# Kernel tuning notes

Hardware: AMD Instinct MI355X
Metric: run time of the kernel (lower is better)

The kernel has to match this reference:

```python
import jax, jax.numpy as jnp
import numpy as np

N_NODES = 100000
N_EDGES = 600000
N_CLASS = 26
HIDDEN = 128


def setup_inputs() -> dict:
    key = jax.random.key(0)
    ks = jax.random.split(key, 8)
    x = jax.random.normal(ks[0], (N_NODES, N_CLASS), dtype=jnp.float32)
    edge_index = jax.random.randint(ks[1], (2, N_EDGES), 0, N_NODES, dtype=jnp.int64)
    edge_weight = jax.random.uniform(ks[2], (N_EDGES,), dtype=jnp.float32)
    W1 = jax.random.normal(ks[3], (N_CLASS, HIDDEN), dtype=jnp.float32) * (1.0 / np.sqrt(N_CLASS))
    b1 = jnp.zeros((HIDDEN,), dtype=jnp.float32)
    W2 = jax.random.normal(ks[4], (HIDDEN, HIDDEN), dtype=jnp.float32) * (1.0 / np.sqrt(HIDDEN))
    b2 = jnp.zeros((HIDDEN,), dtype=jnp.float32)
    Wfc = jax.random.normal(ks[5], (HIDDEN, N_CLASS), dtype=jnp.float32) * (1.0 / np.sqrt(HIDDEN))
    bfc = jnp.zeros((N_CLASS,), dtype=jnp.float32)
    return {"x": x, "edge_index": edge_index, "edge_weight": edge_weight,
            "W1": W1, "b1": b1, "W2": W2, "b2": b2, "Wfc": Wfc, "bfc": bfc}


def _gcn_norm(edge_index, edge_weight, n_nodes):
    # PyG gcn_norm: add self-loops (weight 1), symmetric deg^-1/2 normalization.
    loop = jnp.arange(n_nodes, dtype=edge_index.dtype)
    row = jnp.concatenate([edge_index[0], loop])  # source
    col = jnp.concatenate([edge_index[1], loop])  # destination
    w = jnp.concatenate([edge_weight, jnp.ones((n_nodes,), edge_weight.dtype)])
    deg = jax.ops.segment_sum(w, col, num_segments=n_nodes)
    d_inv_sqrt = jnp.where(deg > 0, jax.lax.rsqrt(jnp.maximum(deg, 1e-12)), 0.0)
    norm = d_inv_sqrt[row] * w * d_inv_sqrt[col]
    return row, col, norm


def _gcn_conv(x, row, col, norm, W, b, n_nodes):
    h = x @ W                              # [N, out]
    msg = norm[:, None] * h[row]           # gather + scale, [E+N, out]
    out = jax.ops.segment_sum(msg, col, num_segments=n_nodes)  # scatter-add
    return out + b


def reference(x, edge_index, edge_weight, W1, b1, W2, b2, Wfc, bfc):
    n = x.shape[0]
    row, col, norm = _gcn_norm(edge_index, edge_weight, n)
    h = jax.nn.relu(_gcn_conv(x, row, col, norm, W1, b1, n))
    h = jax.nn.relu(_gcn_conv(h, row, col, norm, W2, b2, n))
    return h @ Wfc + bfc
```

## Files before the change

### kernel.cpp

```cpp
#include <hip/hip_runtime.h>

#define NNODES 100000
#define NEDGES 600000
#define NCLASS 26
#define HID    128

#define SHIFT  9
#define BCOLS  512
#define NBKT   196
#define EPB    1024
#define NBE    586
#define NH     (NBKT * NBE)

typedef __attribute__((ext_vector_type(8))) short bf16x8;
typedef __attribute__((ext_vector_type(4))) float f32x4;

__device__ inline unsigned short f2bf(float f) {
    unsigned int u = __float_as_uint(f);
    u += 0x7fffu + ((u >> 16) & 1u);
    return (unsigned short)(u >> 16);
}
__device__ inline unsigned int packbf(float a, float b) {
    return (unsigned int)f2bf(a) | ((unsigned int)f2bf(b) << 16);
}
__device__ inline float2 bfpair(unsigned int p) {
    float2 r;
    r.x = __uint_as_float(p << 16);
    r.y = __uint_as_float(p & 0xffff0000u);
    return r;
}
__device__ inline void fma8(float* a, float w, uint4 g) {
    float2 p;
    p = bfpair(g.x); a[0] = fmaf(w, p.x, a[0]); a[1] = fmaf(w, p.y, a[1]);
    p = bfpair(g.y); a[2] = fmaf(w, p.x, a[2]); a[3] = fmaf(w, p.y, a[3]);
    p = bfpair(g.z); a[4] = fmaf(w, p.x, a[4]); a[5] = fmaf(w, p.y, a[5]);
    p = bfpair(g.w); a[6] = fmaf(w, p.x, a[6]); a[7] = fmaf(w, p.y, a[7]);
}
__device__ inline void set8(float* a, uint4 g) {
    float2 p;
    p = bfpair(g.x); a[0] = p.x; a[1] = p.y;
    p = bfpair(g.y); a[2] = p.x; a[3] = p.y;
    p = bfpair(g.z); a[4] = p.x; a[5] = p.y;
    p = bfpair(g.w); a[6] = p.x; a[7] = p.y;
}

__global__ __launch_bounds__(256) void histA_k(const int* __restrict__ col,
                                               int* __restrict__ H) {
    __shared__ int h[NBKT];
    int t = threadIdx.x;
    for (int i = t; i < NBKT; i += 256) h[i] = 0;
    __syncthreads();
    int base = blockIdx.x * EPB;
#pragma unroll
    for (int u = 0; u < 4; u++) {
        int e = base + t + u * 256;
        if (e < NEDGES) atomicAdd(&h[col[e] >> SHIFT], 1);
    }
    __syncthreads();
    for (int i = t; i < NBKT; i += 256) H[i * NBE + blockIdx.x] = h[i];
}

__global__ void scanH1_k(const int* __restrict__ in, int* __restrict__ incl,
                         int* __restrict__ aux, int n) {
    __shared__ int s[256];
    int t = threadIdx.x, gi = blockIdx.x * 256 + t;
    s[t] = (gi < n) ? in[gi] : 0;
    __syncthreads();
    for (int off = 1; off < 256; off <<= 1) {
        int x = (t >= off) ? s[t - off] : 0;
        __syncthreads();
        s[t] += x;
        __syncthreads();
    }
    if (gi < n) incl[gi] = s[t];
    if (t == 255) aux[blockIdx.x] = s[255];
}

__global__ void scan2_k(int* __restrict__ aux, int n) {
    __shared__ int s[512];
    int t = threadIdx.x;
    s[t] = (t < n) ? aux[t] : 0;
    __syncthreads();
    for (int off = 1; off < 512; off <<= 1) {
        int x = (t >= off) ? s[t - off] : 0;
        __syncthreads();
        s[t] += x;
        __syncthreads();
    }
    if (t < n) aux[t] = s[t];
}

__device__ inline int exoff(const int* __restrict__ incl, const int* __restrict__ H,
                            const int* __restrict__ aux, int gi) {
    int add = (gi >= 256) ? aux[(gi >> 8) - 1] : 0;
    return incl[gi] - H[gi] + add;
}

__global__ __launch_bounds__(256) void partB_k(const int* __restrict__ row,
                                               const int* __restrict__ col,
                                               const float* __restrict__ w,
                                               const int* __restrict__ incl,
                                               const int* __restrict__ H,
                                               const int* __restrict__ aux,
                                               uint2* __restrict__ rw,
                                               unsigned short* __restrict__ lc) {
    __shared__ int off[NBKT];
    __shared__ int cur[NBKT];
    int t = threadIdx.x;
    for (int i = t; i < NBKT; i += 256) {
        off[i] = exoff(incl, H, aux, i * NBE + blockIdx.x);
        cur[i] = 0;
    }
    __syncthreads();
    int base = blockIdx.x * EPB;
#pragma unroll
    for (int u = 0; u < 4; u++) {
        int e = base + t + u * 256;
        if (e < NEDGES) {
            int c = col[e], b = c >> SHIFT;
            int p = off[b] + atomicAdd(&cur[b], 1);
            rw[p] = make_uint2((unsigned int)row[e], __float_as_uint(w[e]));
            lc[p] = (unsigned short)(c & (BCOLS - 1));
        }
    }
}

__global__ __launch_bounds__(256) void segbp_k(const uint2* __restrict__ rw,
                                               const unsigned short* __restrict__ lc,
                                               const int* __restrict__ incl,
                                               const int* __restrict__ H,
                                               const int* __restrict__ aux,
                                               int* __restrict__ rowptr,
                                               float* __restrict__ dis,
                                               uint2* __restrict__ meta) {
    __shared__ int   cnt[BCOLS];
    __shared__ float ws[BCOLS];
    __shared__ int   rpl[BCOLS];
    __shared__ int   ps[256];
    int b = blockIdx.x, t = threadIdx.x;
    int c0 = b << SHIFT;
    int ncols = min(BCOLS, NNODES - c0);
    for (int i = t; i < BCOLS; i += 256) { cnt[i] = 0; ws[i] = 0.f; }
    __syncthreads();
    int s    = exoff(incl, H, aux, b * NBE);
    int eend = (b == NBKT - 1) ? NEDGES : exoff(incl, H, aux, (b + 1) * NBE);
    for (int e = s + t; e < eend; e += 256) {
        uint2 m = rw[e];
        int l = lc[e];
        atomicAdd(&cnt[l], 1);
        atomicAdd(&ws[l], __uint_as_float(m.y));
    }
    __syncthreads();
    for (int i = t; i < ncols; i += 256) dis[c0 + i] = rsqrtf(1.0f + ws[i]);
    int a0 = cnt[2 * t], a1 = cnt[2 * t + 1];
    ps[t] = a0 + a1;
    __syncthreads();
    for (int off = 1; off < 256; off <<= 1) {
        int x = (t >= off) ? ps[t - off] : 0;
        __syncthreads();
        ps[t] += x;
        __syncthreads();
    }
    int ex = (t > 0) ? ps[t - 1] : 0;
    rpl[2 * t]     = s + ex;
    rpl[2 * t + 1] = s + ex + a0;
    if (2 * t     < ncols) rowptr[c0 + 2 * t]     = s + ex;
    if (2 * t + 1 < ncols) rowptr[c0 + 2 * t + 1] = s + ex + a0;
    if (b == NBKT - 1 && t == 0) rowptr[NNODES] = NEDGES;
    cnt[2 * t] = 0; cnt[2 * t + 1] = 0;
    __syncthreads();
    for (int e = s + t; e < eend; e += 256) {
        uint2 m = rw[e];
        int l = lc[e];
        int pos = rpl[l] + atomicAdd(&cnt[l], 1);
        meta[pos] = make_uint2(m.x, m.y);
    }
}

__global__ __launch_bounds__(256) void prep_k(const float* __restrict__ W2,
                                              const float* __restrict__ W1,
                                              const float* __restrict__ Wfc,
                                              const float* __restrict__ x,
                                              const float* __restrict__ dis,
                                              unsigned short* __restrict__ wt,
                                              unsigned short* __restrict__ w1t,
                                              unsigned short* __restrict__ wfct,
                                              unsigned int* __restrict__ xp) {
    int b = blockIdx.x, t = threadIdx.x;
    if (b < 64) {
        int idx = b * 256 + t;
        int c = idx >> 7, k = idx & 127;
        wt[c * 128 + k] = f2bf(W2[k * 128 + c]);
    } else if (b < 80) {
        int idx = (b - 64) * 256 + t;
        int c = idx >> 5, k = idx & 31;
        w1t[c * 32 + k] = (k < NCLASS) ? f2bf(W1[k * 128 + c]) : (unsigned short)0;
    } else if (b < 96) {
        int idx = (b - 80) * 256 + t;
        int c = idx >> 7, k = idx & 127;
        wfct[c * 128 + k] = (c < NCLASS) ? f2bf(Wfc[k * NCLASS + c]) : (unsigned short)0;
    } else {
        int i = (b - 96) * 256 + t;
        if (i < NNODES * 16) {
            int r = i >> 4, u = i & 15, f0 = u * 2;
            float d = dis[r];
            float a = (f0     < NCLASS) ? x[r * NCLASS + f0]     : 0.f;
            float c = (f0 + 1 < NCLASS) ? x[r * NCLASS + f0 + 1] : 0.f;
            xp[i] = packbf(d * a, d * c);
        }
    }
}

__global__ __launch_bounds__(256) void agg26_k(const int* __restrict__ rowptr,
                                               const uint2* __restrict__ meta,
                                               const unsigned int* __restrict__ xp,
                                               const float* __restrict__ dis,
                                               unsigned int* __restrict__ aggx) {
    int node = blockIdx.x * 16 + (threadIdx.x >> 4);
    int lane = threadIdx.x & 15;

    float2 acc = bfpair(xp[node * 16 + lane]);
    int j = rowptr[node], jend = rowptr[node + 1];
    for (; j + 3 < jend; j += 4) {
        uint2 m0 = meta[j],     m1 = meta[j + 1];
        uint2 m2 = meta[j + 2], m3 = meta[j + 3];
        unsigned int g0 = xp[m0.x * 16 + lane];
        unsigned int g1 = xp[m1.x * 16 + lane];
        unsigned int g2 = xp[m2.x * 16 + lane];
        unsigned int g3 = xp[m3.x * 16 + lane];
        float v0 = __uint_as_float(m0.y), v1 = __uint_as_float(m1.y);
        float v2 = __uint_as_float(m2.y), v3 = __uint_as_float(m3.y);
        float2 a;
        a = bfpair(g0); acc.x = fmaf(v0, a.x, acc.x); acc.y = fmaf(v0, a.y, acc.y);
        a = bfpair(g1); acc.x = fmaf(v1, a.x, acc.x); acc.y = fmaf(v1, a.y, acc.y);
        a = bfpair(g2); acc.x = fmaf(v2, a.x, acc.x); acc.y = fmaf(v2, a.y, acc.y);
        a = bfpair(g3); acc.x = fmaf(v3, a.x, acc.x); acc.y = fmaf(v3, a.y, acc.y);
    }
    for (; j < jend; j++) {
        uint2 m = meta[j];
        float v = __uint_as_float(m.y);
        float2 a = bfpair(xp[m.x * 16 + lane]);
        acc.x = fmaf(v, a.x, acc.x); acc.y = fmaf(v, a.y, acc.y);
    }
    float d = dis[node];
    aggx[node * 16 + lane] = packbf(d * acc.x, d * acc.y);
}

__global__ __launch_bounds__(256) void gemm12_k(const unsigned short* __restrict__ aggx,
                                                const unsigned short* __restrict__ w1t,
                                                const float* __restrict__ b1,
                                                const unsigned short* __restrict__ wt,
                                                const float* __restrict__ dis,
                                                unsigned short* __restrict__ C, int N) {
    __shared__ unsigned short h1s[128 * 136];
    __shared__ unsigned short Ws[128 * 72];
    const int tid  = threadIdx.x;
    const int wave = tid >> 6, lane = tid & 63;
    const int quad = lane >> 4, l16 = lane & 15;
    const int wm = wave >> 1, wn = wave & 1;
    const int row0 = blockIdx.x * 128;

    bf16x8 a1[4], bw1[4];
#pragma unroll
    for (int t = 0; t < 4; t++) {
        int r = row0 + wm * 64 + t * 16 + l16;
        a1[t] = (r < N) ? *(const bf16x8*)&aggx[(size_t)r * 32 + quad * 8]
                        : (bf16x8)(short)0;
        bw1[t] = *(const bf16x8*)&w1t[(wn * 64 + t * 16 + l16) * 32 + quad * 8];
    }
#pragma unroll
    for (int jj = 0; jj < 4; jj++) {
        int idx = tid + jj * 256;
        int r = idx >> 3, ku = idx & 7;
        *(uint4*)&Ws[r * 72 + ku * 8] = *(const uint4*)&wt[(size_t)r * 128 + ku * 8];
    }
    float b1v[4];
#pragma unroll
    for (int tn = 0; tn < 4; tn++) b1v[tn] = b1[wn * 64 + tn * 16 + l16];
#pragma unroll
    for (int tm = 0; tm < 4; tm++) {
#pragma unroll
        for (int tn = 0; tn < 4; tn++) {
            f32x4 hacc = __builtin_amdgcn_mfma_f32_16x16x32_bf16(
                a1[tm], bw1[tn], (f32x4)0.f, 0, 0, 0);
            int rl = wm * 64 + tm * 16 + quad * 4;
            int col = wn * 64 + tn * 16 + l16;
#pragma unroll
            for (int r = 0; r < 4; r++)
                h1s[(rl + r) * 136 + col] = f2bf(fmaxf(hacc[r] + b1v[tn], 0.f));
        }
    }
    __syncthreads();

    f32x4 acc[4][4];
#pragma unroll
    for (int i = 0; i < 4; i++)
#pragma unroll
        for (int j = 0; j < 4; j++) acc[i][j] = (f32x4)0.f;

    for (int c = 0; c < 2; c++) {
        if (c == 1) {
            __syncthreads();
#pragma unroll
            for (int jj = 0; jj < 4; jj++) {
                int idx = tid + jj * 256;
                int r = idx >> 3, ku = idx & 7;
                *(uint4*)&Ws[r * 72 + ku * 8] =
                    *(const uint4*)&wt[(size_t)r * 128 + 64 + ku * 8];
            }
            __syncthreads();
        }
#pragma unroll
        for (int kc = 0; kc < 2; kc++) {
            const int klA = c * 64 + kc * 32 + quad * 8;
            const int klW = kc * 32 + quad * 8;
            bf16x8 af[4], bfr[4];
#pragma unroll
            for (int t = 0; t < 4; t++) {
                af[t]  = *(const bf16x8*)&h1s[(wm * 64 + t * 16 + l16) * 136 + klA];
                bfr[t] = *(const bf16x8*)&Ws[(wn * 64 + t * 16 + l16) * 72 + klW];
            }
#pragma unroll
            for (int tm = 0; tm < 4; tm++)
#pragma unroll
                for (int tn = 0; tn < 4; tn++)
                    acc[tm][tn] = __builtin_amdgcn_mfma_f32_16x16x32_bf16(
                        af[tm], bfr[tn], acc[tm][tn], 0, 0, 0);
        }
    }

#pragma unroll
    for (int tm = 0; tm < 4; tm++) {
        const int rbase = row0 + wm * 64 + tm * 16 + quad * 4;
        float dv[4];
#pragma unroll
        for (int r = 0; r < 4; r++)
            dv[r] = (rbase + r < N) ? dis[rbase + r] : 0.f;
#pragma unroll
        for (int tn = 0; tn < 4; tn++) {
            const int col = wn * 64 + tn * 16 + l16;
#pragma unroll
            for (int r = 0; r < 4; r++) {
                if (rbase + r < N)
                    C[(size_t)(rbase + r) * 128 + col] = f2bf(dv[r] * acc[tm][tn][r]);
            }
        }
    }
}

__global__ __launch_bounds__(256) void aggfc_k(const int* __restrict__ rowptr,
                                               const uint2* __restrict__ meta,
                                               const unsigned short* __restrict__ h,
                                               const float* __restrict__ dis,
                                               const float* __restrict__ b2,
                                               const unsigned short* __restrict__ wfct,
                                               const float* __restrict__ bfc,
                                               float* __restrict__ out, int N) {
    const int tid = threadIdx.x;
    const int wv = tid >> 6, lane = tid & 63;
    const int q = lane >> 4, m = lane & 15;
    const int nbase = blockIdx.x * 64 + wv * 16;
    const int node = nbase + m;
    const bool valid = node < N;

    float acc[4][8];
    if (valid) {
        const uint4* self = (const uint4*)&h[(size_t)node * 128];
#pragma unroll
        for (int ks = 0; ks < 4; ks++) set8(acc[ks], self[ks * 4 + q]);
    } else {
#pragma unroll
        for (int ks = 0; ks < 4; ks++)
#pragma unroll
            for (int jj = 0; jj < 8; jj++) acc[ks][jj] = 0.f;
    }

    int j = valid ? rowptr[node] : 0;
    int jend = valid ? rowptr[node + 1] : 0;
    for (; j + 1 < jend; j += 2) {
        uint2 m0 = meta[j], m1 = meta[j + 1];
        const uint4* s0 = (const uint4*)&h[(size_t)m0.x * 128];
        const uint4* s1 = (const uint4*)&h[(size_t)m1.x * 128];
        uint4 g0[4], g1[4];
#pragma unroll
        for (int ks = 0; ks < 4; ks++) { g0[ks] = s0[ks * 4 + q]; g1[ks] = s1[ks * 4 + q]; }
        float w0 = __uint_as_float(m0.y), w1 = __uint_as_float(m1.y);
#pragma unroll
        for (int ks = 0; ks < 4; ks++) { fma8(acc[ks], w0, g0[ks]); fma8(acc[ks], w1, g1[ks]); }
    }
    if (j < jend) {
        uint2 mt = meta[j];
        const uint4* s0 = (const uint4*)&h[(size_t)mt.x * 128];
        float w0 = __uint_as_float(mt.y);
#pragma unroll
        for (int ks = 0; ks < 4; ks++) fma8(acc[ks], w0, s0[ks * 4 + q]);
    }

    float d = valid ? dis[node] : 0.f;
    bf16x8 af[4];
#pragma unroll
    for (int ks = 0; ks < 4; ks++) {
        const float4* bp = (const float4*)&b2[ks * 32 + q * 8];
        float4 bA = bp[0], bB = bp[1];
        union { bf16x8 v; unsigned short s[8]; } u;
        u.s[0] = f2bf(fmaxf(fmaf(d, acc[ks][0], bA.x), 0.f));
        u.s[1] = f2bf(fmaxf(fmaf(d, acc[ks][1], bA.y), 0.f));
        u.s[2] = f2bf(fmaxf(fmaf(d, acc[ks][2], bA.z), 0.f));
        u.s[3] = f2bf(fmaxf(fmaf(d, acc[ks][3], bA.w), 0.f));
        u.s[4] = f2bf(fmaxf(fmaf(d, acc[ks][4], bB.x), 0.f));
        u.s[5] = f2bf(fmaxf(fmaf(d, acc[ks][5], bB.y), 0.f));
        u.s[6] = f2bf(fmaxf(fmaf(d, acc[ks][6], bB.z), 0.f));
        u.s[7] = f2bf(fmaxf(fmaf(d, acc[ks][7], bB.w), 0.f));
        af[ks] = u.v;
    }

#pragma unroll
    for (int n = 0; n < 2; n++) {
        f32x4 o = (f32x4)0.f;
#pragma unroll
        for (int ks = 0; ks < 4; ks++) {
            bf16x8 bfr = *(const bf16x8*)&wfct[(size_t)(n * 16 + m) * 128 + ks * 32 + q * 8];
            o = __builtin_amdgcn_mfma_f32_16x16x32_bf16(af[ks], bfr, o, 0, 0, 0);
        }
        int col = n * 16 + m;
        if (col < NCLASS) {
            float bv = bfc[col];
            int r0 = nbase + q * 4;
#pragma unroll
            for (int r = 0; r < 4; r++) {
                if (r0 + r < N)
                    out[(size_t)(r0 + r) * NCLASS + col] = o[r] + bv;
            }
        }
    }
}

extern "C" void kernel_launch(void* const* d_in, const int* in_sizes, int n_in,
                              void* d_out, int out_size, void* d_ws, size_t ws_size,
                              hipStream_t stream) {
    const float* x   = (const float*)d_in[0];
    const int*   ei  = (const int*)d_in[1];
    const float* ew  = (const float*)d_in[2];
    const float* W1  = (const float*)d_in[3];
    const float* b1  = (const float*)d_in[4];
    const float* W2  = (const float*)d_in[5];
    const float* b2  = (const float*)d_in[6];
    const float* Wfc = (const float*)d_in[7];
    const float* bfc = (const float*)d_in[8];
    float* out = (float*)d_out;

    const int N = NNODES;
    const int* erow = ei;
    const int* ecol = ei + NEDGES;

    float* fws    = (float*)d_ws;
    float* dis    = fws;
    int*   rowptr = (int*)(fws + 100000);
    int*   H      = (int*)(fws + 200004);
    int*   incl   = (int*)(fws + 314860);
    int*   aux    = (int*)(fws + 429716);
    uint2* rw     = (uint2*)(fws + 430228);
    unsigned short* lc = (unsigned short*)(fws + 1630228);
    uint2* meta   = (uint2*)(fws + 1930228);
    unsigned short* wt16   = (unsigned short*)(fws + 3130228);
    unsigned short* w1t16  = (unsigned short*)(fws + 3138420);
    unsigned short* wfct16 = (unsigned short*)(fws + 3140468);
    unsigned int*   xp     = (unsigned int*)(fws + 3142516);
    unsigned int*   aggx   = (unsigned int*)(fws + 4742516);
    unsigned short* hB16   = (unsigned short*)(fws + 6342516);

    const int gScan = (NH + 255) / 256;
    const int g128  = (N + 127) / 128;
    const int gA26  = N / 16;
    const int gPrep = 96 + (N * 16 + 255) / 256;
    const int gFc   = (N + 63) / 64;

    histA_k<<<NBE, 256, 0, stream>>>(ecol, H);
    scanH1_k<<<gScan, 256, 0, stream>>>(H, incl, aux, NH);
    scan2_k<<<1, 512, 0, stream>>>(aux, gScan);
    partB_k<<<NBE, 256, 0, stream>>>(erow, ecol, ew, incl, H, aux, rw, lc);
    segbp_k<<<NBKT, 256, 0, stream>>>(rw, lc, incl, H, aux, rowptr, dis, meta);

    prep_k<<<gPrep, 256, 0, stream>>>(W2, W1, Wfc, x, dis, wt16, w1t16, wfct16, xp);

    agg26_k<<<gA26, 256, 0, stream>>>(rowptr, meta, xp, dis, aggx);
    gemm12_k<<<g128, 256, 0, stream>>>((const unsigned short*)aggx, w1t16, b1,
                                       wt16, dis, hB16, N);

    aggfc_k<<<gFc, 256, 0, stream>>>(rowptr, meta, hB16, dis, b2, wfct16, bfc, out, N);
}
```

Measured before the change: 213.8 us.

## Fuse layer-1 aggregation into GEMM kernel and restructure layer-2 gather via LDS

Removes the separate agg26 kernel by performing the 26-feature neighbor aggregation inside gemm12_k, staging it in shared memory (reusing the h1s buffer) before the MFMA chain. This drops one launch and the aggx global round-trip. In aggfc_k, the per-node gather now uses 32 lanes per node with 8-byte loads and a 4-edge unroll, in place of 16 lanes with 64-byte chunks. Results go through an LDS tile before the final MFMA. This trades register pressure for more lanes per node, but the fused gemm kernel now has a serial gather phase with only 782 blocks.

```diff
diff --git a/kernel.cpp b/kernel.cpp
--- a/kernel.cpp
+++ b/kernel.cpp
@@ -28,20 +28,6 @@
     r.x = __uint_as_float(p << 16);
     r.y = __uint_as_float(p & 0xffff0000u);
     return r;
-}
-__device__ inline void fma8(float* a, float w, uint4 g) {
-    float2 p;
-    p = bfpair(g.x); a[0] = fmaf(w, p.x, a[0]); a[1] = fmaf(w, p.y, a[1]);
-    p = bfpair(g.y); a[2] = fmaf(w, p.x, a[2]); a[3] = fmaf(w, p.y, a[3]);
-    p = bfpair(g.z); a[4] = fmaf(w, p.x, a[4]); a[5] = fmaf(w, p.y, a[5]);
-    p = bfpair(g.w); a[6] = fmaf(w, p.x, a[6]); a[7] = fmaf(w, p.y, a[7]);
-}
-__device__ inline void set8(float* a, uint4 g) {
-    float2 p;
-    p = bfpair(g.x); a[0] = p.x; a[1] = p.y;
-    p = bfpair(g.y); a[2] = p.x; a[3] = p.y;
-    p = bfpair(g.z); a[4] = p.x; a[5] = p.y;
-    p = bfpair(g.w); a[6] = p.x; a[7] = p.y;
 }
 
 __global__ __launch_bounds__(256) void histA_k(const int* __restrict__ col,
@@ -211,61 +197,68 @@
     }
 }
 
-__global__ __launch_bounds__(256) void agg26_k(const int* __restrict__ rowptr,
-                                               const uint2* __restrict__ meta,
-                                               const unsigned int* __restrict__ xp,
-                                               const float* __restrict__ dis,
-                                               unsigned int* __restrict__ aggx) {
-    int node = blockIdx.x * 16 + (threadIdx.x >> 4);
-    int lane = threadIdx.x & 15;
-
-    float2 acc = bfpair(xp[node * 16 + lane]);
-    int j = rowptr[node], jend = rowptr[node + 1];
-    for (; j + 3 < jend; j += 4) {
-        uint2 m0 = meta[j],     m1 = meta[j + 1];
-        uint2 m2 = meta[j + 2], m3 = meta[j + 3];
-        unsigned int g0 = xp[m0.x * 16 + lane];
-        unsigned int g1 = xp[m1.x * 16 + lane];
-        unsigned int g2 = xp[m2.x * 16 + lane];
-        unsigned int g3 = xp[m3.x * 16 + lane];
-        float v0 = __uint_as_float(m0.y), v1 = __uint_as_float(m1.y);
-        float v2 = __uint_as_float(m2.y), v3 = __uint_as_float(m3.y);
-        float2 a;
-        a = bfpair(g0); acc.x = fmaf(v0, a.x, acc.x); acc.y = fmaf(v0, a.y, acc.y);
-        a = bfpair(g1); acc.x = fmaf(v1, a.x, acc.x); acc.y = fmaf(v1, a.y, acc.y);
-        a = bfpair(g2); acc.x = fmaf(v2, a.x, acc.x); acc.y = fmaf(v2, a.y, acc.y);
-        a = bfpair(g3); acc.x = fmaf(v3, a.x, acc.x); acc.y = fmaf(v3, a.y, acc.y);
-    }
-    for (; j < jend; j++) {
-        uint2 m = meta[j];
-        float v = __uint_as_float(m.y);
-        float2 a = bfpair(xp[m.x * 16 + lane]);
-        acc.x = fmaf(v, a.x, acc.x); acc.y = fmaf(v, a.y, acc.y);
-    }
-    float d = dis[node];
-    aggx[node * 16 + lane] = packbf(d * acc.x, d * acc.y);
-}
-
-__global__ __launch_bounds__(256) void gemm12_k(const unsigned short* __restrict__ aggx,
+__global__ __launch_bounds__(256) void gemm12_k(const int* __restrict__ rowptr,
+                                                const uint2* __restrict__ meta,
+                                                const unsigned int* __restrict__ xp,
+                                                const float* __restrict__ dis,
                                                 const unsigned short* __restrict__ w1t,
                                                 const float* __restrict__ b1,
                                                 const unsigned short* __restrict__ wt,
-                                                const float* __restrict__ dis,
                                                 unsigned short* __restrict__ C, int N) {
     __shared__ unsigned short h1s[128 * 136];
     __shared__ unsigned short Ws[128 * 72];
+    unsigned int* axs = (unsigned int*)h1s;
     const int tid  = threadIdx.x;
     const int wave = tid >> 6, lane = tid & 63;
     const int quad = lane >> 4, l16 = lane & 15;
     const int wm = wave >> 1, wn = wave & 1;
     const int row0 = blockIdx.x * 128;
 
+    {
+        const int ln = tid & 15;
+        const int ng = tid >> 4;
+#pragma unroll 2
+        for (int p = 0; p < 8; p++) {
+            int r = p * 16 + ng;
+            int node = row0 + r;
+            float2 acc = make_float2(0.f, 0.f);
+            if (node < N) {
+                acc = bfpair(xp[node * 16 + ln]);
+                int j = rowptr[node], jend = rowptr[node + 1];
+                for (; j + 3 < jend; j += 4) {
+                    uint2 m0 = meta[j],     m1 = meta[j + 1];
+                    uint2 m2 = meta[j + 2], m3 = meta[j + 3];
+                    unsigned int g0 = xp[m0.x * 16 + ln];
+                    unsigned int g1 = xp[m1.x * 16 + ln];
+                    unsigned int g2 = xp[m2.x * 16 + ln];
+                    unsigned int g3 = xp[m3.x * 16 + ln];
+                    float v0 = __uint_as_float(m0.y), v1 = __uint_as_float(m1.y);
+                    float v2 = __uint_as_float(m2.y), v3 = __uint_as_float(m3.y);
+                    float2 a;
+                    a = bfpair(g0); acc.x = fmaf(v0, a.x, acc.x); acc.y = fmaf(v0, a.y, acc.y);
+                    a = bfpair(g1); acc.x = fmaf(v1, a.x, acc.x); acc.y = fmaf(v1, a.y, acc.y);
+                    a = bfpair(g2); acc.x = fmaf(v2, a.x, acc.x); acc.y = fmaf(v2, a.y, acc.y);
+                    a = bfpair(g3); acc.x = fmaf(v3, a.x, acc.x); acc.y = fmaf(v3, a.y, acc.y);
+                }
+                for (; j < jend; j++) {
+                    uint2 m = meta[j];
+                    float v = __uint_as_float(m.y);
+                    float2 a = bfpair(xp[m.x * 16 + ln]);
+                    acc.x = fmaf(v, a.x, acc.x); acc.y = fmaf(v, a.y, acc.y);
+                }
+                float d = dis[node];
+                acc.x *= d; acc.y *= d;
+            }
+            axs[r * 20 + ln] = packbf(acc.x, acc.y);
+        }
+    }
+    __syncthreads();
+
     bf16x8 a1[4], bw1[4];
 #pragma unroll
     for (int t = 0; t < 4; t++) {
-        int r = row0 + wm * 64 + t * 16 + l16;
-        a1[t] = (r < N) ? *(const bf16x8*)&aggx[(size_t)r * 32 + quad * 8]
-                        : (bf16x8)(short)0;
+        int r = wm * 64 + t * 16 + l16;
+        a1[t]  = *(const bf16x8*)((const unsigned short*)axs + r * 40 + quad * 8);
         bw1[t] = *(const bf16x8*)&w1t[(wn * 64 + t * 16 + l16) * 32 + quad * 8];
     }
 #pragma unroll
@@ -277,6 +270,7 @@
     float b1v[4];
 #pragma unroll
     for (int tn = 0; tn < 4; tn++) b1v[tn] = b1[wn * 64 + tn * 16 + l16];
+    __syncthreads();
 #pragma unroll
     for (int tm = 0; tm < 4; tm++) {
 #pragma unroll
@@ -350,69 +344,78 @@
 
 __global__ __launch_bounds__(256) void aggfc_k(const int* __restrict__ rowptr,
                                                const uint2* __restrict__ meta,
-                                               const unsigned short* __restrict__ h,
+                                               const uint2* __restrict__ h,
                                                const float* __restrict__ dis,
                                                const float* __restrict__ b2,
                                                const unsigned short* __restrict__ wfct,
                                                const float* __restrict__ bfc,
                                                float* __restrict__ out, int N) {
+    __shared__ unsigned short h2s[64 * 136];
     const int tid = threadIdx.x;
     const int wv = tid >> 6, lane = tid & 63;
+    const int l32 = lane & 31, sub = lane >> 5;
+    const int nbase = blockIdx.x * 64;
+
+#pragma unroll 2
+    for (int p = 0; p < 8; p++) {
+        int r = p * 8 + wv * 2 + sub;
+        int node = nbase + r;
+        float4 acc = make_float4(0.f, 0.f, 0.f, 0.f);
+        float d = 0.f;
+        if (node < N) {
+            d = dis[node];
+            uint2 hcu = h[(size_t)node * 32 + l32];
+            float2 h0 = bfpair(hcu.x), h1 = bfpair(hcu.y);
+            acc.x = h0.x; acc.y = h0.y; acc.z = h1.x; acc.w = h1.y;
+            int j = rowptr[node], jend = rowptr[node + 1];
+            for (; j + 3 < jend; j += 4) {
+                uint2 m0 = meta[j],     m1 = meta[j + 1];
+                uint2 m2 = meta[j + 2], m3 = meta[j + 3];
+                uint2 g0 = h[(size_t)m0.x * 32 + l32];
+                uint2 g1 = h[(size_t)m1.x * 32 + l32];
+                uint2 g2 = h[(size_t)m2.x * 32 + l32];
+                uint2 g3 = h[(size_t)m3.x * 32 + l32];
+                float v0 = __uint_as_float(m0.y), v1 = __uint_as_float(m1.y);
+                float v2 = __uint_as_float(m2.y), v3 = __uint_as_float(m3.y);
+                float2 a, b;
+                a = bfpair(g0.x); b = bfpair(g0.y);
+                acc.x = fmaf(v0, a.x, acc.x); acc.y = fmaf(v0, a.y, acc.y);
+                acc.z = fmaf(v0, b.x, acc.z); acc.w = fmaf(v0, b.y, acc.w);
+                a = bfpair(g1.x); b = bfpair(g1.y);
+                acc.x = fmaf(v1, a.x, acc.x); acc.y = fmaf(v1, a.y, acc.y);
+                acc.z = fmaf(v1, b.x, acc.z); acc.w = fmaf(v1, b.y, acc.w);
+                a = bfpair(g2.x); b = bfpair(g2.y);
+                acc.x = fmaf(v2, a.x, acc.x); acc.y = fmaf(v2, a.y, acc.y);
+                acc.z = fmaf(v2, b.x, acc.z); acc.w = fmaf(v2, b.y, acc.w);
+                a = bfpair(g3.x); b = bfpair(g3.y);
+                acc.x = fmaf(v3, a.x, acc.x); acc.y = fmaf(v3, a.y, acc.y);
+                acc.z = fmaf(v3, b.x, acc.z); acc.w = fmaf(v3, b.y, acc.w);
+            }
+            for (; j < jend; j++) {
+                uint2 m = meta[j];
+                float v = __uint_as_float(m.y);
+                uint2 g = h[(size_t)m.x * 32 + l32];
+                float2 a = bfpair(g.x), b = bfpair(g.y);
+                acc.x = fmaf(v, a.x, acc.x); acc.y = fmaf(v, a.y, acc.y);
+                acc.z = fmaf(v, b.x, acc.z); acc.w = fmaf(v, b.y, acc.w);
+            }
+        }
+        float4 bv = ((const float4*)b2)[l32];
+        acc.x = fmaxf(fmaf(d, acc.x, bv.x), 0.f);
+        acc.y = fmaxf(fmaf(d, acc.y, bv.y), 0.f);
+        acc.z = fmaxf(fmaf(d, acc.z, bv.z), 0.f);
+        acc.w = fmaxf(fmaf(d, acc.w, bv.w), 0.f);
+        if (node >= N) { acc = make_float4(0.f, 0.f, 0.f, 0.f); }
+        *(uint2*)&h2s[r * 136 + l32 * 4] =
+            make_uint2(packbf(acc.x, acc.y), packbf(acc.z, acc.w));
+    }
+    __syncthreads();
+
     const int q = lane >> 4, m = lane & 15;
-    const int nbase = blockIdx.x * 64 + wv * 16;
-    const int node = nbase + m;
-    const bool valid = node < N;
-
-    float acc[4][8];
-    if (valid) {
-        const uint4* self = (const uint4*)&h[(size_t)node * 128];
-#pragma unroll
-        for (int ks = 0; ks < 4; ks++) set8(acc[ks], self[ks * 4 + q]);
-    } else {
-#pragma unroll
-        for (int ks = 0; ks < 4; ks++)
-#pragma unroll
-            for (int jj = 0; jj < 8; jj++) acc[ks][jj] = 0.f;
-    }
-
-    int j = valid ? rowptr[node] : 0;
-    int jend = valid ? rowptr[node + 1] : 0;
-    for (; j + 1 < jend; j += 2) {
-        uint2 m0 = meta[j], m1 = meta[j + 1];
-        const uint4* s0 = (const uint4*)&h[(size_t)m0.x * 128];
-        const uint4* s1 = (const uint4*)&h[(size_t)m1.x * 128];
-        uint4 g0[4], g1[4];
-#pragma unroll
-        for (int ks = 0; ks < 4; ks++) { g0[ks] = s0[ks * 4 + q]; g1[ks] = s1[ks * 4 + q]; }
-        float w0 = __uint_as_float(m0.y), w1 = __uint_as_float(m1.y);
-#pragma unroll
-        for (int ks = 0; ks < 4; ks++) { fma8(acc[ks], w0, g0[ks]); fma8(acc[ks], w1, g1[ks]); }
-    }
-    if (j < jend) {
-        uint2 mt = meta[j];
-        const uint4* s0 = (const uint4*)&h[(size_t)mt.x * 128];
-        float w0 = __uint_as_float(mt.y);
-#pragma unroll
-        for (int ks = 0; ks < 4; ks++) fma8(acc[ks], w0, s0[ks * 4 + q]);
-    }
-
-    float d = valid ? dis[node] : 0.f;
     bf16x8 af[4];
 #pragma unroll
-    for (int ks = 0; ks < 4; ks++) {
-        const float4* bp = (const float4*)&b2[ks * 32 + q * 8];
-        float4 bA = bp[0], bB = bp[1];
-        union { bf16x8 v; unsigned short s[8]; } u;
-        u.s[0] = f2bf(fmaxf(fmaf(d, acc[ks][0], bA.x), 0.f));
-        u.s[1] = f2bf(fmaxf(fmaf(d, acc[ks][1], bA.y), 0.f));
-        u.s[2] = f2bf(fmaxf(fmaf(d, acc[ks][2], bA.z), 0.f));
-        u.s[3] = f2bf(fmaxf(fmaf(d, acc[ks][3], bA.w), 0.f));
-        u.s[4] = f2bf(fmaxf(fmaf(d, acc[ks][4], bB.x), 0.f));
-        u.s[5] = f2bf(fmaxf(fmaf(d, acc[ks][5], bB.y), 0.f));
-        u.s[6] = f2bf(fmaxf(fmaf(d, acc[ks][6], bB.z), 0.f));
-        u.s[7] = f2bf(fmaxf(fmaf(d, acc[ks][7], bB.w), 0.f));
-        af[ks] = u.v;
-    }
+    for (int ks = 0; ks < 4; ks++)
+        af[ks] = *(const bf16x8*)&h2s[(wv * 16 + m) * 136 + ks * 32 + q * 8];
 
 #pragma unroll
     for (int n = 0; n < 2; n++) {
@@ -425,7 +428,7 @@
         int col = n * 16 + m;
         if (col < NCLASS) {
             float bv = bfc[col];
-            int r0 = nbase + q * 4;
+            int r0 = nbase + wv * 16 + q * 4;
 #pragma unroll
             for (int r = 0; r < 4; r++) {
                 if (r0 + r < N)
@@ -466,12 +469,10 @@
     unsigned short* w1t16  = (unsigned short*)(fws + 3138420);
     unsigned short* wfct16 = (unsigned short*)(fws + 3140468);
     unsigned int*   xp     = (unsigned int*)(fws + 3142516);
-    unsigned int*   aggx   = (unsigned int*)(fws + 4742516);
-    unsigned short* hB16   = (unsigned short*)(fws + 6342516);
+    unsigned short* hB16   = (unsigned short*)(fws + 4742516);
 
     const int gScan = (NH + 255) / 256;
     const int g128  = (N + 127) / 128;
-    const int gA26  = N / 16;
     const int gPrep = 96 + (N * 16 + 255) / 256;
     const int gFc   = (N + 63) / 64;
 
@@ -483,9 +484,8 @@
 
     prep_k<<<gPrep, 256, 0, stream>>>(W2, W1, Wfc, x, dis, wt16, w1t16, wfct16, xp);
 
-    agg26_k<<<gA26, 256, 0, stream>>>(rowptr, meta, xp, dis, aggx);
-    gemm12_k<<<g128, 256, 0, stream>>>((const unsigned short*)aggx, w1t16, b1,
-                                       wt16, dis, hB16, N);
-
-    aggfc_k<<<gFc, 256, 0, stream>>>(rowptr, meta, hB16, dis, b2, wfct16, bfc, out, N);
-}
+    gemm12_k<<<g128, 256, 0, stream>>>(rowptr, meta, xp, dis, w1t16, b1, wt16, hB16, N);
+
+    aggfc_k<<<gFc, 256, 0, stream>>>(rowptr, meta, (const uint2*)hB16, dis, b2,
+                                     wfct16, bfc, out, N);
+}
```

New measurement: 238.5 us. 11.6% more time.
